# Kernel optimization log

Hardware: AMD Instinct MI355X
Metric: run time of the kernel (lower is better)

The kernel has to match this reference:

```python
import jax, jax.numpy as jnp
import numpy as np

N = 50000
E = 800000
G = 2500  # number of graphs


def setup_inputs() -> dict:
    key = jax.random.key(0)
    ks = jax.random.split(key, 10)
    x = jax.random.normal(ks[0], (N, 128), dtype=jnp.float32)
    edge_index = jax.random.randint(ks[1], (2, E), 0, N, dtype=jnp.int64)
    batch = jnp.sort(jax.random.randint(ks[2], (N,), 0, G, dtype=jnp.int64))
    def lin(k, fan_in, shape):
        return jax.random.normal(k, shape, dtype=jnp.float32) / np.sqrt(fan_in)
    return {
        'x': x, 'edge_index': edge_index, 'batch': batch,
        'W1': lin(ks[3], 128, (128, 64)), 'b1': jnp.zeros((64,), jnp.float32),
        'W2': lin(ks[4], 64, (64, 64)),  'b2': jnp.zeros((64,), jnp.float32),
        'W3': lin(ks[5], 64, (64, 64)),  'b3': jnp.zeros((64,), jnp.float32),
        'Wp1': lin(ks[6], 64, (64, 64)), 'bp1': jnp.zeros((64,), jnp.float32),
        'Wp2': lin(ks[7], 64, (64, 32)), 'bp2': jnp.zeros((32,), jnp.float32),
    }


def _gcn_norm(edge_index, n_nodes):
    # PyG GCNConv default: add self-loops, symmetric normalization
    loops = jnp.arange(n_nodes, dtype=edge_index.dtype)
    src = jnp.concatenate([edge_index[0], loops])
    dst = jnp.concatenate([edge_index[1], loops])
    deg = jax.ops.segment_sum(jnp.ones_like(dst, dtype=jnp.float32), dst,
                              num_segments=n_nodes)
    dis = jnp.where(deg > 0, jax.lax.rsqrt(deg), 0.0)
    norm = dis[src] * dis[dst]  # [E + N]
    return src, dst, norm


def _gcn_conv(x, W, b, src, dst, norm, n_nodes):
    h = x @ W                                   # transform first (small dim)
    m = h[src] * norm[:, None]                  # gather + scale
    out = jax.ops.segment_sum(m, dst, num_segments=n_nodes)  # scatter-add
    return out + b


def reference(x, edge_index, batch, W1, b1, W2, b2, W3, b3, Wp1, bp1, Wp2, bp2):
    n_nodes = x.shape[0]
    src, dst, norm = _gcn_norm(edge_index, n_nodes)
    x1 = jax.nn.relu(_gcn_conv(x, W1, b1, src, dst, norm, n_nodes))
    x2 = jax.nn.relu(_gcn_conv(x1, W2, b2, src, dst, norm, n_nodes))
    x3 = jax.nn.relu(_gcn_conv(x2, W3, b3, src, dst, norm, n_nodes))
    h = x1 + x2 + x3
    # global_mean_pool
    sums = jax.ops.segment_sum(h, batch, num_segments=G)
    counts = jax.ops.segment_sum(jnp.ones((n_nodes,), jnp.float32), batch,
                                 num_segments=G)
    pooled = sums / jnp.maximum(counts, 1.0)[:, None]
    z = jax.nn.relu(pooled @ Wp1 + bp1) @ Wp2 + bp2
    return z
```

## Files before the change

kernel.cpp:

```cpp
#include <hip/hip_runtime.h>
#include <math.h>


typedef short short8 __attribute__((ext_vector_type(8)));
typedef float f32x4 __attribute__((ext_vector_type(4)));

__device__ inline float bf2f(unsigned short h) {
    return __uint_as_float((unsigned)h << 16);
}
__device__ inline unsigned short f2bf(float f) {
    unsigned u = __float_as_uint(f);
    return (unsigned short)((u + (0x7FFFu + ((u >> 16) & 1u))) >> 16);
}
__device__ inline void bh8f(short8 u, float4& a, float4& b) {
    a.x = bf2f((unsigned short)u[0]); a.y = bf2f((unsigned short)u[1]);
    a.z = bf2f((unsigned short)u[2]); a.w = bf2f((unsigned short)u[3]);
    b.x = bf2f((unsigned short)u[4]); b.y = bf2f((unsigned short)u[5]);
    b.z = bf2f((unsigned short)u[6]); b.w = bf2f((unsigned short)u[7]);
}
__device__ inline float4 f4add(float4 a, float4 acc) {
    acc.x += a.x; acc.y += a.y; acc.z += a.z; acc.w += a.w;
    return acc;
}

template <int K>
__global__ __launch_bounds__(256) void k_hist_gemm(const int* __restrict__ dst,
                                                   int* __restrict__ hist, int E, int chunk,
                                                   const float* __restrict__ X,
                                                   const float* __restrict__ W,
                                                   unsigned short* __restrict__ H, int n) {
    __shared__ int hh[256];
    __shared__ short wt[64 * K];
    int t = threadIdx.x;
    if (blockIdx.x < 256) {
        hh[t] = 0;
        __syncthreads();
        int e0 = blockIdx.x * chunk;
        int e1 = min(e0 + chunk, E);
        for (int e = e0 + t; e < e1; e += 256) atomicAdd(&hh[dst[e] >> 8], 1);
        __syncthreads();
        hist[blockIdx.x * 256 + t] = hh[t];
        return;
    }
    for (int idx = t; idx < 64 * K; idx += 256) {
        int k = idx >> 6, ch = idx & 63;
        wt[ch * K + k] = (short)f2bf(W[idx]);
    }
    __syncthreads();
    int wave = t >> 6, lane = t & 63;
    int q = lane >> 4, l = lane & 15;
    int tile = (blockIdx.x - 256) * 4 + wave;
    if (tile * 16 >= n) return;
    int node = tile * 16 + l;
    short8 afr[4][K / 32];
#pragma unroll
    for (int mb = 0; mb < 4; mb++)
#pragma unroll
        for (int s = 0; s < K / 32; s++)
            afr[mb][s] = *(const short8*)(wt + (mb * 16 + l) * K + s * 32 + q * 8);
    f32x4 acc[4] = {};
    const float* xr = X + (size_t)node * K + q * 8;
#pragma unroll
    for (int s = 0; s < K / 32; s++) {
        float4 xa = *(const float4*)(xr + s * 32);
        float4 xb = *(const float4*)(xr + s * 32 + 4);
        short8 bfr;
        bfr[0] = (short)f2bf(xa.x); bfr[1] = (short)f2bf(xa.y);
        bfr[2] = (short)f2bf(xa.z); bfr[3] = (short)f2bf(xa.w);
        bfr[4] = (short)f2bf(xb.x); bfr[5] = (short)f2bf(xb.y);
        bfr[6] = (short)f2bf(xb.z); bfr[7] = (short)f2bf(xb.w);
#pragma unroll
        for (int mb = 0; mb < 4; mb++)
            acc[mb] = __builtin_amdgcn_mfma_f32_16x16x32_bf16(afr[mb][s], bfr, acc[mb], 0, 0, 0);
    }
#pragma unroll
    for (int mb = 0; mb < 4; mb++) {
        ushort4 u;
        u.x = f2bf(acc[mb][0]); u.y = f2bf(acc[mb][1]);
        u.z = f2bf(acc[mb][2]); u.w = f2bf(acc[mb][3]);
        ((ushort4*)H)[(size_t)node * 16 + mb * 4 + q] = u;
    }
}

__global__ void kA_colscan(const int* __restrict__ hist, int* __restrict__ cursorA,
                           int* __restrict__ tot) {
    __shared__ int s[256];
    int t = threadIdx.x;
    int k = blockIdx.x;
    int v = hist[t * 256 + k];
    s[t] = v;
    __syncthreads();
    for (int st = 1; st < 256; st <<= 1) {
        int u = s[t];
        if (t >= st) u += s[t - st];
        __syncthreads();
        s[t] = u;
        __syncthreads();
    }
    cursorA[t * 256 + k] = s[t] - v;
    if (t == 255) tot[k] = s[255];
}

__global__ void kA_scatter(const int* __restrict__ src, const int* __restrict__ dst,
                           const int* __restrict__ cursorA, const int* __restrict__ tot,
                           unsigned* __restrict__ ebuf, int E, int chunk) {
    __shared__ int s[256];
    __shared__ int cur[256];
    int t = threadIdx.x;
    s[t] = tot[t];
    __syncthreads();
    for (int st = 1; st < 256; st <<= 1) {
        int u = s[t];
        if (t >= st) u += s[t - st];
        __syncthreads();
        s[t] = u;
        __syncthreads();
    }
    int bstart = (t == 0) ? 0 : s[t - 1];
    cur[t] = cursorA[blockIdx.x * 256 + t] + bstart;
    __syncthreads();
    int e0 = blockIdx.x * chunk;
    int e1 = min(e0 + chunk, E);
    for (int e = e0 + t; e < e1; e += 256) {
        int d = dst[e];
        int p = atomicAdd(&cur[d >> 8], 1);
        ebuf[p] = ((unsigned)(d & 255) << 24) | (unsigned)src[e];
    }
}

__global__ void kB(const unsigned* __restrict__ ebuf, const int* __restrict__ tot,
                   float* __restrict__ dis, int* __restrict__ offsP,
                   unsigned* __restrict__ col, unsigned short* __restrict__ Hb,
                   unsigned short* __restrict__ Hb2, int N, int ZR) {
    __shared__ int s[256];
    __shared__ int h[256];
    __shared__ int cur[256];
    __shared__ float sdis[256];
    int t = threadIdx.x;
    int k = blockIdx.x;
    s[t] = tot[t];
    __syncthreads();
    for (int st = 1; st < 256; st <<= 1) {
        int u = s[t];
        if (t >= st) u += s[t - st];
        __syncthreads();
        s[t] = u;
        __syncthreads();
    }
    int lo = (k == 0) ? 0 : s[k - 1];
    int hi = s[k];
    int padbase = ((lo + 3) & ~3) + 768 * k;
    h[t] = 0;
    __syncthreads();
    for (int p = lo + t; p < hi; p += 256) atomicAdd(&h[ebuf[p] >> 24], 1);
    __syncthreads();
    int c = h[t];
    int cp = (c + 3) & ~3;
    int node = k * 256 + t;
    float dn = rsqrtf((float)(c + 1));
    sdis[t] = dn;
    if (node < N) dis[node] = dn;
    s[t] = cp;
    __syncthreads();
    for (int st = 1; st < 256; st <<= 1) {
        int u = s[t];
        if (t >= st) u += s[t - st];
        __syncthreads();
        s[t] = u;
        __syncthreads();
    }
    int start = padbase + s[t] - cp;
    if (node < N) offsP[node] = (start << 9) | cp;
    cur[t] = start;
    __syncthreads();
    for (int p = lo + t; p < hi; p += 256) {
        unsigned e = ebuf[p];
        int q = atomicAdd(&cur[e >> 24], 1);
        col[q] = e & 0x00FFFFFFu;
    }
    __syncthreads();
    if (node < N) {
        int end = start + cp;
        for (int q = cur[t]; q < end; q++) col[q] = (unsigned)ZR;
    }
    for (int idx = t; idx < 2048; idx += 256) {
        int nl = idx >> 3, cs = idx & 7;
        int nd = k * 256 + nl;
        if (nd >= N) continue;
        float d2 = sdis[nl];
        short8 v = ((const short8*)Hb)[(size_t)nd * 8 + cs];
        float4 a, b;
        bh8f(v, a, b);
        short8 o;
        o[0] = (short)f2bf(a.x * d2); o[1] = (short)f2bf(a.y * d2);
        o[2] = (short)f2bf(a.z * d2); o[3] = (short)f2bf(a.w * d2);
        o[4] = (short)f2bf(b.x * d2); o[5] = (short)f2bf(b.y * d2);
        o[6] = (short)f2bf(b.z * d2); o[7] = (short)f2bf(b.w * d2);
        ((short8*)Hb)[(size_t)nd * 8 + cs] = o;
    }
    if (k == 0) {
        if (t < 32) ((unsigned*)Hb)[(size_t)ZR * 32 + t] = 0u;
        else if (t < 64) ((unsigned*)Hb2)[(size_t)ZR * 32 + (t - 32)] = 0u;
    }
}

__global__ __launch_bounds__(256) void k_aggemm(const unsigned short* __restrict__ H,
                                                const unsigned* __restrict__ col,
                                                const int* __restrict__ offsP,
                                                const float* __restrict__ dis,
                                                const float* __restrict__ bias,
                                                const float* __restrict__ W,
                                                unsigned short* __restrict__ Xout,
                                                unsigned short* __restrict__ Hout, int n) {
    __shared__ short wt[64 * 64];
    __shared__ short vbuf[32 * 72];
    int t = threadIdx.x;
    for (int idx = t; idx < 64 * 64; idx += 256) {
        int k = idx >> 6, ch = idx & 63;
        wt[ch * 64 + k] = (short)f2bf(W[idx]);
    }
    const short8* Hs = (const short8*)H;
    int base = blockIdx.x * 32;
    int cs = t & 7;
    int nl = t >> 3;
    int node = base + nl;
    const float4* bias4 = (const float4*)bias;
    float4 bb0 = bias4[cs * 2];
    float4 bb1 = bias4[cs * 2 + 1];
    if (node < n) {
        float dn = dis[node];
        float4 acc0, acc1;
        bh8f(Hs[(size_t)node * 8 + cs], acc0, acc1);
        int po = offsP[node];
        int p = po >> 9, hiP = p + (po & 511);
        for (; p + 8 <= hiP; p += 8) {
            uint4 ea = *(const uint4*)(col + p);
            uint4 eb = *(const uint4*)(col + p + 4);
            short8 g0 = Hs[(size_t)ea.x * 8 + cs];
            short8 g1 = Hs[(size_t)ea.y * 8 + cs];
            short8 g2 = Hs[(size_t)ea.z * 8 + cs];
            short8 g3 = Hs[(size_t)ea.w * 8 + cs];
            short8 g4 = Hs[(size_t)eb.x * 8 + cs];
            short8 g5 = Hs[(size_t)eb.y * 8 + cs];
            short8 g6 = Hs[(size_t)eb.z * 8 + cs];
            short8 g7 = Hs[(size_t)eb.w * 8 + cs];
            float4 a, b;
            bh8f(g0, a, b); acc0 = f4add(a, acc0); acc1 = f4add(b, acc1);
            bh8f(g1, a, b); acc0 = f4add(a, acc0); acc1 = f4add(b, acc1);
            bh8f(g2, a, b); acc0 = f4add(a, acc0); acc1 = f4add(b, acc1);
            bh8f(g3, a, b); acc0 = f4add(a, acc0); acc1 = f4add(b, acc1);
            bh8f(g4, a, b); acc0 = f4add(a, acc0); acc1 = f4add(b, acc1);
            bh8f(g5, a, b); acc0 = f4add(a, acc0); acc1 = f4add(b, acc1);
            bh8f(g6, a, b); acc0 = f4add(a, acc0); acc1 = f4add(b, acc1);
            bh8f(g7, a, b); acc0 = f4add(a, acc0); acc1 = f4add(b, acc1);
        }
        if (p < hiP) {
            uint4 e4 = *(const uint4*)(col + p);
            short8 g0 = Hs[(size_t)e4.x * 8 + cs];
            short8 g1 = Hs[(size_t)e4.y * 8 + cs];
            short8 g2 = Hs[(size_t)e4.z * 8 + cs];
            short8 g3 = Hs[(size_t)e4.w * 8 + cs];
            float4 a, b;
            bh8f(g0, a, b); acc0 = f4add(a, acc0); acc1 = f4add(b, acc1);
            bh8f(g1, a, b); acc0 = f4add(a, acc0); acc1 = f4add(b, acc1);
            bh8f(g2, a, b); acc0 = f4add(a, acc0); acc1 = f4add(b, acc1);
            bh8f(g3, a, b); acc0 = f4add(a, acc0); acc1 = f4add(b, acc1);
        }
        float4 v0, v1;
        v0.x = fmaxf(acc0.x * dn + bb0.x, 0.f);
        v0.y = fmaxf(acc0.y * dn + bb0.y, 0.f);
        v0.z = fmaxf(acc0.z * dn + bb0.z, 0.f);
        v0.w = fmaxf(acc0.w * dn + bb0.w, 0.f);
        v1.x = fmaxf(acc1.x * dn + bb1.x, 0.f);
        v1.y = fmaxf(acc1.y * dn + bb1.y, 0.f);
        v1.z = fmaxf(acc1.z * dn + bb1.z, 0.f);
        v1.w = fmaxf(acc1.w * dn + bb1.w, 0.f);
        short8 o;
        o[0] = (short)f2bf(v0.x); o[1] = (short)f2bf(v0.y);
        o[2] = (short)f2bf(v0.z); o[3] = (short)f2bf(v0.w);
        o[4] = (short)f2bf(v1.x); o[5] = (short)f2bf(v1.y);
        o[6] = (short)f2bf(v1.z); o[7] = (short)f2bf(v1.w);
        ((short8*)Xout)[(size_t)node * 8 + cs] = o;
        *(short8*)(vbuf + nl * 72 + cs * 8) = o;
    }
    __syncthreads();
    int wave = t >> 6, lane = t & 63;
    if (wave >= 2) return;
    int q = lane >> 4, l = lane & 15;
    if (base + wave * 16 >= n) return;
    int mnode = base + wave * 16 + l;
    float dn2 = dis[mnode];
    short8 afr[4][2];
#pragma unroll
    for (int mb = 0; mb < 4; mb++)
#pragma unroll
        for (int s = 0; s < 2; s++)
            afr[mb][s] = *(const short8*)(wt + (mb * 16 + l) * 64 + s * 32 + q * 8);
    f32x4 acc[4] = {};
#pragma unroll
    for (int s = 0; s < 2; s++) {
        short8 bfr = *(const short8*)(vbuf + (wave * 16 + l) * 72 + s * 32 + q * 8);
#pragma unroll
        for (int mb = 0; mb < 4; mb++)
            acc[mb] = __builtin_amdgcn_mfma_f32_16x16x32_bf16(afr[mb][s], bfr, acc[mb], 0, 0, 0);
    }
#pragma unroll
    for (int mb = 0; mb < 4; mb++) {
        ushort4 u;
        u.x = f2bf(acc[mb][0] * dn2); u.y = f2bf(acc[mb][1] * dn2);
        u.z = f2bf(acc[mb][2] * dn2); u.w = f2bf(acc[mb][3] * dn2);
        ((ushort4*)Hout)[(size_t)mnode * 16 + mb * 4 + q] = u;
    }
}

__global__ void k_agg3(const unsigned short* __restrict__ H, const unsigned* __restrict__ col,
                       const int* __restrict__ offsP, const float* __restrict__ dis,
                       const float* __restrict__ bias,
                       const unsigned short* __restrict__ add1,
                       const unsigned short* __restrict__ add2,
                       float* __restrict__ OutS, int n) {
    int t = threadIdx.x;
    int node = blockIdx.x * 32 + (t >> 3);
    if (node >= n) return;
    int lane = t & 7;
    const short8* Hs = (const short8*)H;
    float dn = dis[node];
    float4 acc0, acc1;
    bh8f(Hs[(size_t)node * 8 + lane], acc0, acc1);
    int po = offsP[node];
    int p = po >> 9, hiP = p + (po & 511);
    for (; p + 8 <= hiP; p += 8) {
        uint4 ea = *(const uint4*)(col + p);
        uint4 eb = *(const uint4*)(col + p + 4);
        short8 g0 = Hs[(size_t)ea.x * 8 + lane];
        short8 g1 = Hs[(size_t)ea.y * 8 + lane];
        short8 g2 = Hs[(size_t)ea.z * 8 + lane];
        short8 g3 = Hs[(size_t)ea.w * 8 + lane];
        short8 g4 = Hs[(size_t)eb.x * 8 + lane];
        short8 g5 = Hs[(size_t)eb.y * 8 + lane];
        short8 g6 = Hs[(size_t)eb.z * 8 + lane];
        short8 g7 = Hs[(size_t)eb.w * 8 + lane];
        float4 a, b;
        bh8f(g0, a, b); acc0 = f4add(a, acc0); acc1 = f4add(b, acc1);
        bh8f(g1, a, b); acc0 = f4add(a, acc0); acc1 = f4add(b, acc1);
        bh8f(g2, a, b); acc0 = f4add(a, acc0); acc1 = f4add(b, acc1);
        bh8f(g3, a, b); acc0 = f4add(a, acc0); acc1 = f4add(b, acc1);
        bh8f(g4, a, b); acc0 = f4add(a, acc0); acc1 = f4add(b, acc1);
        bh8f(g5, a, b); acc0 = f4add(a, acc0); acc1 = f4add(b, acc1);
        bh8f(g6, a, b); acc0 = f4add(a, acc0); acc1 = f4add(b, acc1);
        bh8f(g7, a, b); acc0 = f4add(a, acc0); acc1 = f4add(b, acc1);
    }
    if (p < hiP) {
        uint4 e4 = *(const uint4*)(col + p);
        short8 g0 = Hs[(size_t)e4.x * 8 + lane];
        short8 g1 = Hs[(size_t)e4.y * 8 + lane];
        short8 g2 = Hs[(size_t)e4.z * 8 + lane];
        short8 g3 = Hs[(size_t)e4.w * 8 + lane];
        float4 a, b;
        bh8f(g0, a, b); acc0 = f4add(a, acc0); acc1 = f4add(b, acc1);
        bh8f(g1, a, b); acc0 = f4add(a, acc0); acc1 = f4add(b, acc1);
        bh8f(g2, a, b); acc0 = f4add(a, acc0); acc1 = f4add(b, acc1);
        bh8f(g3, a, b); acc0 = f4add(a, acc0); acc1 = f4add(b, acc1);
    }
    const float4* bias4 = (const float4*)bias;
    float4 bb0 = bias4[lane * 2];
    float4 bb1 = bias4[lane * 2 + 1];
    float4 v0, v1;
    v0.x = fmaxf(acc0.x * dn + bb0.x, 0.f);
    v0.y = fmaxf(acc0.y * dn + bb0.y, 0.f);
    v0.z = fmaxf(acc0.z * dn + bb0.z, 0.f);
    v0.w = fmaxf(acc0.w * dn + bb0.w, 0.f);
    v1.x = fmaxf(acc1.x * dn + bb1.x, 0.f);
    v1.y = fmaxf(acc1.y * dn + bb1.y, 0.f);
    v1.z = fmaxf(acc1.z * dn + bb1.z, 0.f);
    v1.w = fmaxf(acc1.w * dn + bb1.w, 0.f);
    size_t slot = (size_t)node * 8 + lane;
    float4 a10, a11, a20, a21;
    bh8f(((const short8*)add1)[slot], a10, a11);
    bh8f(((const short8*)add2)[slot], a20, a21);
    v0.x += a10.x + a20.x; v0.y += a10.y + a20.y;
    v0.z += a10.z + a20.z; v0.w += a10.w + a20.w;
    v1.x += a11.x + a21.x; v1.y += a11.y + a21.y;
    v1.z += a11.z + a21.z; v1.w += a11.w + a21.w;
    float4* S4 = (float4*)OutS;
    size_t oi = (size_t)node * 16 + (size_t)lane * 2;
    S4[oi] = v0;
    S4[oi + 1] = v1;
}

__global__ void k_poolhead(const float* __restrict__ S, const int* __restrict__ batch,
                           const float* __restrict__ Wp1, const float* __restrict__ bp1,
                           const float* __restrict__ Wp2, const float* __restrict__ bp2,
                           float* __restrict__ out, int n, int G) {
    int g = blockIdx.x;
    int j = threadIdx.x;
    int a = 0, b = n;
    while (a < b) { int m = (a + b) >> 1; if (batch[m] < g) a = m + 1; else b = m; }
    int beg = a;
    b = n;
    while (a < b) { int m = (a + b) >> 1; if (batch[m] < g + 1) a = m + 1; else b = m; }
    int end = a;
    float sum = 0.f;
    int i = beg;
    for (; i + 2 <= end; i += 2)
        sum += S[(size_t)i * 64 + j] + S[(size_t)(i + 1) * 64 + j];
    if (i < end) sum += S[(size_t)i * 64 + j];
    float cnt = (float)(end - beg);
    float p = sum / fmaxf(cnt, 1.f);
    __shared__ float ps[64];
    __shared__ float ts[64];
    ps[j] = p;
    __syncthreads();
    float t1 = bp1[j];
#pragma unroll 8
    for (int k = 0; k < 64; k++) t1 += ps[k] * Wp1[k * 64 + j];
    t1 = fmaxf(t1, 0.f);
    ts[j] = t1;
    __syncthreads();
    if (j < 32) {
        float o = bp2[j];
#pragma unroll 8
        for (int k = 0; k < 64; k++) o += ts[k] * Wp2[k * 32 + j];
        out[(size_t)g * 32 + j] = o;
    }
}

extern "C" void kernel_launch(void* const* d_in, const int* in_sizes, int n_in,
                              void* d_out, int out_size, void* d_ws, size_t ws_size,
                              hipStream_t stream) {
    const float* x   = (const float*)d_in[0];
    const int*   ei  = (const int*)d_in[1];
    const int*   bat = (const int*)d_in[2];
    const float* W1  = (const float*)d_in[3];
    const float* b1  = (const float*)d_in[4];
    const float* W2  = (const float*)d_in[5];
    const float* b2  = (const float*)d_in[6];
    const float* W3  = (const float*)d_in[7];
    const float* b3  = (const float*)d_in[8];
    const float* Wp1 = (const float*)d_in[9];
    const float* bp1 = (const float*)d_in[10];
    const float* Wp2 = (const float*)d_in[11];
    const float* bp2 = (const float*)d_in[12];

    int N = in_sizes[0] / 128;
    int E = in_sizes[1] / 2;
    int G = out_size / 32;
    const int* src = ei;
    const int* dst = ei + E;

    char* w = (char*)d_ws;
    auto alloc = [&](size_t bytes) -> void* {
        void* p = (void*)w;
        w += (bytes + 255) & ~(size_t)255;
        return p;
    };
    int NB = (N + 255) / 256;
    int ZR = N;
    int*            offsP   = (int*)alloc((size_t)N * 4);
    unsigned*       col     = (unsigned*)alloc(((size_t)E + 3 * (size_t)N + 2048) * 4);
    float*          dis     = (float*)alloc((size_t)N * 4);
    int*            hist    = (int*)alloc((size_t)256 * 256 * 4);
    int*            cursorA = (int*)alloc((size_t)256 * 256 * 4);
    int*            tot     = (int*)alloc((size_t)256 * 4);
    unsigned*       ebuf    = (unsigned*)alloc((size_t)E * 4);
    unsigned short* Hb      = (unsigned short*)alloc(((size_t)N + 16) * 64 * 2);
    unsigned short* Hb2     = (unsigned short*)alloc(((size_t)N + 16) * 64 * 2);
    unsigned short* X1      = (unsigned short*)alloc((size_t)N * 64 * 2);
    unsigned short* X2      = (unsigned short*)alloc((size_t)N * 64 * 2);
    float*          S       = (float*)alloc((size_t)N * 64 * 4);

    int chunk = (E + 255) / 256;
    int ggemm = ((N >> 4) + 3) / 4;
    int gfuse = (N + 31) / 32;
    int gagg  = (N + 31) / 32;

    k_hist_gemm<128><<<256 + ggemm, 256, 0, stream>>>(dst, hist, E, chunk, x, W1, Hb, N);
    kA_colscan<<<256, 256, 0, stream>>>(hist, cursorA, tot);
    kA_scatter<<<256, 256, 0, stream>>>(src, dst, cursorA, tot, ebuf, E, chunk);
    kB<<<NB, 256, 0, stream>>>(ebuf, tot, dis, offsP, col, Hb, Hb2, N, ZR);

    k_aggemm<<<gfuse, 256, 0, stream>>>(Hb, col, offsP, dis, b1, W2, X1, Hb2, N);
    k_aggemm<<<gfuse, 256, 0, stream>>>(Hb2, col, offsP, dis, b2, W3, X2, Hb, N);
    k_agg3<<<gagg, 256, 0, stream>>>(Hb, col, offsP, dis, b3, X1, X2, S, N);

    k_poolhead<<<G, 64, 0, stream>>>(S, bat, Wp1, bp1, Wp2, bp2, (float*)d_out, N, G);
}
```

Measured before the change: 215.5 us.

## Merge preprocessing kernels into one cooperative kernel with grid syncs

Replaces the four CSR-build and first-GEMM kernels with a single cooperative kernel of 512 blocks that uses grid-wide syncs between the histogram/GEMM, column scan, scatter and bucket-sort phases. The aim is to remove kernel launch gaps and tail effects between the small preprocessing stages. The histogram now uses 512 edge chunks, and each scan thread handles two chunks. This adds the cost of grid barriers and needs all 512 blocks, each with 16KB of LDS for W1, to be co-resident.

```diff
diff --git a/kernel.cpp b/kernel.cpp
--- a/kernel.cpp
+++ b/kernel.cpp
@@ -1,4 +1,5 @@
 #include <hip/hip_runtime.h>
+#include <hip/hip_cooperative_groups.h>
 #include <math.h>
 
 
@@ -23,184 +24,180 @@
     return acc;
 }
 
-template <int K>
-__global__ __launch_bounds__(256) void k_hist_gemm(const int* __restrict__ dst,
-                                                   int* __restrict__ hist, int E, int chunk,
-                                                   const float* __restrict__ X,
-                                                   const float* __restrict__ W,
-                                                   unsigned short* __restrict__ H, int n) {
-    __shared__ int hh[256];
-    __shared__ short wt[64 * K];
-    int t = threadIdx.x;
-    if (blockIdx.x < 256) {
-        hh[t] = 0;
-        __syncthreads();
-        int e0 = blockIdx.x * chunk;
-        int e1 = min(e0 + chunk, E);
-        for (int e = e0 + t; e < e1; e += 256) atomicAdd(&hh[dst[e] >> 8], 1);
-        __syncthreads();
-        hist[blockIdx.x * 256 + t] = hh[t];
-        return;
-    }
-    for (int idx = t; idx < 64 * K; idx += 256) {
-        int k = idx >> 6, ch = idx & 63;
-        wt[ch * K + k] = (short)f2bf(W[idx]);
-    }
-    __syncthreads();
-    int wave = t >> 6, lane = t & 63;
-    int q = lane >> 4, l = lane & 15;
-    int tile = (blockIdx.x - 256) * 4 + wave;
-    if (tile * 16 >= n) return;
-    int node = tile * 16 + l;
-    short8 afr[4][K / 32];
-#pragma unroll
-    for (int mb = 0; mb < 4; mb++)
-#pragma unroll
-        for (int s = 0; s < K / 32; s++)
-            afr[mb][s] = *(const short8*)(wt + (mb * 16 + l) * K + s * 32 + q * 8);
-    f32x4 acc[4] = {};
-    const float* xr = X + (size_t)node * K + q * 8;
-#pragma unroll
-    for (int s = 0; s < K / 32; s++) {
-        float4 xa = *(const float4*)(xr + s * 32);
-        float4 xb = *(const float4*)(xr + s * 32 + 4);
-        short8 bfr;
-        bfr[0] = (short)f2bf(xa.x); bfr[1] = (short)f2bf(xa.y);
-        bfr[2] = (short)f2bf(xa.z); bfr[3] = (short)f2bf(xa.w);
-        bfr[4] = (short)f2bf(xb.x); bfr[5] = (short)f2bf(xb.y);
-        bfr[6] = (short)f2bf(xb.z); bfr[7] = (short)f2bf(xb.w);
-#pragma unroll
-        for (int mb = 0; mb < 4; mb++)
-            acc[mb] = __builtin_amdgcn_mfma_f32_16x16x32_bf16(afr[mb][s], bfr, acc[mb], 0, 0, 0);
-    }
-#pragma unroll
-    for (int mb = 0; mb < 4; mb++) {
-        ushort4 u;
-        u.x = f2bf(acc[mb][0]); u.y = f2bf(acc[mb][1]);
-        u.z = f2bf(acc[mb][2]); u.w = f2bf(acc[mb][3]);
-        ((ushort4*)H)[(size_t)node * 16 + mb * 4 + q] = u;
-    }
-}
-
-__global__ void kA_colscan(const int* __restrict__ hist, int* __restrict__ cursorA,
-                           int* __restrict__ tot) {
-    __shared__ int s[256];
-    int t = threadIdx.x;
-    int k = blockIdx.x;
-    int v = hist[t * 256 + k];
-    s[t] = v;
-    __syncthreads();
-    for (int st = 1; st < 256; st <<= 1) {
-        int u = s[t];
-        if (t >= st) u += s[t - st];
-        __syncthreads();
-        s[t] = u;
-        __syncthreads();
-    }
-    cursorA[t * 256 + k] = s[t] - v;
-    if (t == 255) tot[k] = s[255];
-}
-
-__global__ void kA_scatter(const int* __restrict__ src, const int* __restrict__ dst,
-                           const int* __restrict__ cursorA, const int* __restrict__ tot,
-                           unsigned* __restrict__ ebuf, int E, int chunk) {
-    __shared__ int s[256];
-    __shared__ int cur[256];
-    int t = threadIdx.x;
-    s[t] = tot[t];
-    __syncthreads();
-    for (int st = 1; st < 256; st <<= 1) {
-        int u = s[t];
-        if (t >= st) u += s[t - st];
-        __syncthreads();
-        s[t] = u;
-        __syncthreads();
-    }
-    int bstart = (t == 0) ? 0 : s[t - 1];
-    cur[t] = cursorA[blockIdx.x * 256 + t] + bstart;
-    __syncthreads();
-    int e0 = blockIdx.x * chunk;
-    int e1 = min(e0 + chunk, E);
-    for (int e = e0 + t; e < e1; e += 256) {
-        int d = dst[e];
-        int p = atomicAdd(&cur[d >> 8], 1);
-        ebuf[p] = ((unsigned)(d & 255) << 24) | (unsigned)src[e];
-    }
-}
-
-__global__ void kB(const unsigned* __restrict__ ebuf, const int* __restrict__ tot,
-                   float* __restrict__ dis, int* __restrict__ offsP,
-                   unsigned* __restrict__ col, unsigned short* __restrict__ Hb,
-                   unsigned short* __restrict__ Hb2, int N, int ZR) {
-    __shared__ int s[256];
-    __shared__ int h[256];
+__global__ __launch_bounds__(256) void k_pre(
+    const int* __restrict__ src, const int* __restrict__ dst, int E, int chunk,
+    const float* __restrict__ X, const float* __restrict__ W1,
+    unsigned short* __restrict__ Hb, unsigned short* __restrict__ Hb2,
+    int* __restrict__ hist, int* __restrict__ cursorA, int* __restrict__ tot,
+    unsigned* __restrict__ ebuf, float* __restrict__ dis, int* __restrict__ offsP,
+    unsigned* __restrict__ col, int N, int ZR, int nunits) {
+    __shared__ short wt[64 * 128];
+    __shared__ int sh[256];
+    __shared__ int h2[256];
     __shared__ int cur[256];
     __shared__ float sdis[256];
     int t = threadIdx.x;
-    int k = blockIdx.x;
-    s[t] = tot[t];
+    int b = blockIdx.x;
+    int NBLK = (int)gridDim.x;
+
+    for (int idx = t; idx < 64 * 128; idx += 256) {
+        int k = idx >> 6, ch = idx & 63;
+        wt[ch * 128 + k] = (short)f2bf(W1[idx]);
+    }
+    sh[t] = 0;
     __syncthreads();
-    for (int st = 1; st < 256; st <<= 1) {
-        int u = s[t];
-        if (t >= st) u += s[t - st];
-        __syncthreads();
-        s[t] = u;
-        __syncthreads();
-    }
-    int lo = (k == 0) ? 0 : s[k - 1];
-    int hi = s[k];
-    int padbase = ((lo + 3) & ~3) + 768 * k;
-    h[t] = 0;
+    int e0 = b * chunk;
+    int e1 = min(e0 + chunk, E);
+    for (int e = e0 + t; e < e1; e += 256) atomicAdd(&sh[dst[e] >> 8], 1);
     __syncthreads();
-    for (int p = lo + t; p < hi; p += 256) atomicAdd(&h[ebuf[p] >> 24], 1);
-    __syncthreads();
-    int c = h[t];
-    int cp = (c + 3) & ~3;
-    int node = k * 256 + t;
-    float dn = rsqrtf((float)(c + 1));
-    sdis[t] = dn;
-    if (node < N) dis[node] = dn;
-    s[t] = cp;
-    __syncthreads();
-    for (int st = 1; st < 256; st <<= 1) {
-        int u = s[t];
-        if (t >= st) u += s[t - st];
-        __syncthreads();
-        s[t] = u;
-        __syncthreads();
-    }
-    int start = padbase + s[t] - cp;
-    if (node < N) offsP[node] = (start << 9) | cp;
-    cur[t] = start;
-    __syncthreads();
-    for (int p = lo + t; p < hi; p += 256) {
-        unsigned e = ebuf[p];
-        int q = atomicAdd(&cur[e >> 24], 1);
-        col[q] = e & 0x00FFFFFFu;
-    }
-    __syncthreads();
-    if (node < N) {
-        int end = start + cp;
-        for (int q = cur[t]; q < end; q++) col[q] = (unsigned)ZR;
-    }
-    for (int idx = t; idx < 2048; idx += 256) {
-        int nl = idx >> 3, cs = idx & 7;
-        int nd = k * 256 + nl;
-        if (nd >= N) continue;
-        float d2 = sdis[nl];
-        short8 v = ((const short8*)Hb)[(size_t)nd * 8 + cs];
-        float4 a, b;
-        bh8f(v, a, b);
-        short8 o;
-        o[0] = (short)f2bf(a.x * d2); o[1] = (short)f2bf(a.y * d2);
-        o[2] = (short)f2bf(a.z * d2); o[3] = (short)f2bf(a.w * d2);
-        o[4] = (short)f2bf(b.x * d2); o[5] = (short)f2bf(b.y * d2);
-        o[6] = (short)f2bf(b.z * d2); o[7] = (short)f2bf(b.w * d2);
-        ((short8*)Hb)[(size_t)nd * 8 + cs] = o;
-    }
-    if (k == 0) {
-        if (t < 32) ((unsigned*)Hb)[(size_t)ZR * 32 + t] = 0u;
-        else if (t < 64) ((unsigned*)Hb2)[(size_t)ZR * 32 + (t - 32)] = 0u;
+    hist[b * 256 + t] = sh[t];
+    {
+        int wave = t >> 6, lane = t & 63;
+        int q = lane >> 4, l = lane & 15;
+        for (int unit = b; unit < nunits; unit += NBLK) {
+            int tile = unit * 4 + wave;
+            if (tile * 16 < N) {
+                int node = tile * 16 + l;
+                short8 afr[4][4];
+#pragma unroll
+                for (int mb = 0; mb < 4; mb++)
+#pragma unroll
+                    for (int s = 0; s < 4; s++)
+                        afr[mb][s] = *(const short8*)(wt + (mb * 16 + l) * 128 + s * 32 + q * 8);
+                f32x4 acc[4] = {};
+                const float* xr = X + (size_t)node * 128 + q * 8;
+#pragma unroll
+                for (int s = 0; s < 4; s++) {
+                    float4 xa = *(const float4*)(xr + s * 32);
+                    float4 xb = *(const float4*)(xr + s * 32 + 4);
+                    short8 bfr;
+                    bfr[0] = (short)f2bf(xa.x); bfr[1] = (short)f2bf(xa.y);
+                    bfr[2] = (short)f2bf(xa.z); bfr[3] = (short)f2bf(xa.w);
+                    bfr[4] = (short)f2bf(xb.x); bfr[5] = (short)f2bf(xb.y);
+                    bfr[6] = (short)f2bf(xb.z); bfr[7] = (short)f2bf(xb.w);
+#pragma unroll
+                    for (int mb = 0; mb < 4; mb++)
+                        acc[mb] = __builtin_amdgcn_mfma_f32_16x16x32_bf16(afr[mb][s], bfr, acc[mb], 0, 0, 0);
+                }
+#pragma unroll
+                for (int mb = 0; mb < 4; mb++) {
+                    ushort4 u;
+                    u.x = f2bf(acc[mb][0]); u.y = f2bf(acc[mb][1]);
+                    u.z = f2bf(acc[mb][2]); u.w = f2bf(acc[mb][3]);
+                    ((ushort4*)Hb)[(size_t)node * 16 + mb * 4 + q] = u;
+                }
+            }
+        }
+    }
+    cooperative_groups::this_grid().sync();
+
+    if (b < 256) {
+        int k = b;
+        int v0 = hist[(2 * t) * 256 + k];
+        int v1 = hist[(2 * t + 1) * 256 + k];
+        sh[t] = v0 + v1;
+        __syncthreads();
+        for (int st = 1; st < 256; st <<= 1) {
+            int u = sh[t];
+            if (t >= st) u += sh[t - st];
+            __syncthreads();
+            sh[t] = u;
+            __syncthreads();
+        }
+        int base0 = sh[t] - (v0 + v1);
+        cursorA[(2 * t) * 256 + k] = base0;
+        cursorA[(2 * t + 1) * 256 + k] = base0 + v0;
+        if (t == 255) tot[k] = sh[255];
+    }
+    cooperative_groups::this_grid().sync();
+
+    {
+        sh[t] = tot[t];
+        __syncthreads();
+        for (int st = 1; st < 256; st <<= 1) {
+            int u = sh[t];
+            if (t >= st) u += sh[t - st];
+            __syncthreads();
+            sh[t] = u;
+            __syncthreads();
+        }
+        int bstart = (t == 0) ? 0 : sh[t - 1];
+        cur[t] = cursorA[b * 256 + t] + bstart;
+        __syncthreads();
+        for (int e = e0 + t; e < e1; e += 256) {
+            int d = dst[e];
+            int p = atomicAdd(&cur[d >> 8], 1);
+            ebuf[p] = ((unsigned)(d & 255) << 24) | (unsigned)src[e];
+        }
+    }
+    cooperative_groups::this_grid().sync();
+
+    if (b * 256 >= N) return;
+    {
+        int k = b;
+        sh[t] = tot[t];
+        h2[t] = 0;
+        __syncthreads();
+        for (int st = 1; st < 256; st <<= 1) {
+            int u = sh[t];
+            if (t >= st) u += sh[t - st];
+            __syncthreads();
+            sh[t] = u;
+            __syncthreads();
+        }
+        int lo = (k == 0) ? 0 : sh[k - 1];
+        int hi = sh[k];
+        int padbase = ((lo + 3) & ~3) + 768 * k;
+        for (int p = lo + t; p < hi; p += 256) atomicAdd(&h2[ebuf[p] >> 24], 1);
+        __syncthreads();
+        int c = h2[t];
+        int cp = (c + 3) & ~3;
+        int node = k * 256 + t;
+        float dn = rsqrtf((float)(c + 1));
+        sdis[t] = dn;
+        if (node < N) dis[node] = dn;
+        sh[t] = cp;
+        __syncthreads();
+        for (int st = 1; st < 256; st <<= 1) {
+            int u = sh[t];
+            if (t >= st) u += sh[t - st];
+            __syncthreads();
+            sh[t] = u;
+            __syncthreads();
+        }
+        int start = padbase + sh[t] - cp;
+        if (node < N) offsP[node] = (start << 9) | cp;
+        cur[t] = start;
+        __syncthreads();
+        for (int p = lo + t; p < hi; p += 256) {
+            unsigned e = ebuf[p];
+            int q = atomicAdd(&cur[e >> 24], 1);
+            col[q] = e & 0x00FFFFFFu;
+        }
+        __syncthreads();
+        if (node < N) {
+            int end = start + cp;
+            for (int q = cur[t]; q < end; q++) col[q] = (unsigned)ZR;
+        }
+        for (int idx = t; idx < 2048; idx += 256) {
+            int nl = idx >> 3, cs = idx & 7;
+            int nd = k * 256 + nl;
+            if (nd >= N) continue;
+            float d2 = sdis[nl];
+            short8 v = ((const short8*)Hb)[(size_t)nd * 8 + cs];
+            float4 a, bb;
+            bh8f(v, a, bb);
+            short8 o;
+            o[0] = (short)f2bf(a.x * d2); o[1] = (short)f2bf(a.y * d2);
+            o[2] = (short)f2bf(a.z * d2); o[3] = (short)f2bf(a.w * d2);
+            o[4] = (short)f2bf(bb.x * d2); o[5] = (short)f2bf(bb.y * d2);
+            o[6] = (short)f2bf(bb.z * d2); o[7] = (short)f2bf(bb.w * d2);
+            ((short8*)Hb)[(size_t)nd * 8 + cs] = o;
+        }
+        if (k == 0) {
+            if (t < 32) ((unsigned*)Hb)[(size_t)ZR * 32 + t] = 0u;
+            else if (t < 64) ((unsigned*)Hb2)[(size_t)ZR * 32 + (t - 32)] = 0u;
+        }
     }
 }
 
@@ -454,13 +451,12 @@
         w += (bytes + 255) & ~(size_t)255;
         return p;
     };
-    int NB = (N + 255) / 256;
     int ZR = N;
     int*            offsP   = (int*)alloc((size_t)N * 4);
     unsigned*       col     = (unsigned*)alloc(((size_t)E + 3 * (size_t)N + 2048) * 4);
     float*          dis     = (float*)alloc((size_t)N * 4);
-    int*            hist    = (int*)alloc((size_t)256 * 256 * 4);
-    int*            cursorA = (int*)alloc((size_t)256 * 256 * 4);
+    int*            hist    = (int*)alloc((size_t)512 * 256 * 4);
+    int*            cursorA = (int*)alloc((size_t)512 * 256 * 4);
     int*            tot     = (int*)alloc((size_t)256 * 4);
     unsigned*       ebuf    = (unsigned*)alloc((size_t)E * 4);
     unsigned short* Hb      = (unsigned short*)alloc(((size_t)N + 16) * 64 * 2);
@@ -469,15 +465,20 @@
     unsigned short* X2      = (unsigned short*)alloc((size_t)N * 64 * 2);
     float*          S       = (float*)alloc((size_t)N * 64 * 4);
 
-    int chunk = (E + 255) / 256;
-    int ggemm = ((N >> 4) + 3) / 4;
+    int chunk = (E + 511) / 512;
+    int nunits = (N + 63) / 64;
     int gfuse = (N + 31) / 32;
     int gagg  = (N + 31) / 32;
 
-    k_hist_gemm<128><<<256 + ggemm, 256, 0, stream>>>(dst, hist, E, chunk, x, W1, Hb, N);
-    kA_colscan<<<256, 256, 0, stream>>>(hist, cursorA, tot);
-    kA_scatter<<<256, 256, 0, stream>>>(src, dst, cursorA, tot, ebuf, E, chunk);
-    kB<<<NB, 256, 0, stream>>>(ebuf, tot, dis, offsP, col, Hb, Hb2, N, ZR);
+    {
+        void* args[] = {(void*)&src, (void*)&dst, (void*)&E, (void*)&chunk,
+                        (void*)&x, (void*)&W1, (void*)&Hb, (void*)&Hb2,
+                        (void*)&hist, (void*)&cursorA, (void*)&tot,
+                        (void*)&ebuf, (void*)&dis, (void*)&offsP, (void*)&col,
+                        (void*)&N, (void*)&ZR, (void*)&nunits};
+        hipLaunchCooperativeKernel((const void*)k_pre, dim3(512), dim3(256),
+                                   args, 0, stream);
+    }
 
     k_aggemm<<<gfuse, 256, 0, stream>>>(Hb, col, offsP, dis, b1, W2, X1, Hb2, N);
     k_aggemm<<<gfuse, 256, 0, stream>>>(Hb2, col, offsP, dis, b2, W3, X2, Hb, N);
```

After: 409.5 us. 90.0% more time.

## Fuse mean-pool accumulation into final aggregation kernel via segmented atomics

Applied to the files above, without the earlier changes.

The last GCN aggregation now reduces its per-node outputs within each 32-node block by graph id in shared memory and atomically adds partial sums into a small pooled buffer. This removes the full N×64 fp32 intermediate write and the later re-read in the pooling kernel. The pooled buffer is zeroed inside the column-scan kernel, so no extra launch is needed. It adds float atomics, which make the summation order nondeterministic, and a serial 32-step loop over the block's nodes run by 64 threads after a barrier.

```diff
diff --git a/kernel.cpp b/kernel.cpp
--- a/kernel.cpp
+++ b/kernel.cpp
@@ -83,7 +83,7 @@
 }
 
 __global__ void kA_colscan(const int* __restrict__ hist, int* __restrict__ cursorA,
-                           int* __restrict__ tot) {
+                           int* __restrict__ tot, float* __restrict__ pooled, int PG) {
     __shared__ int s[256];
     int t = threadIdx.x;
     int k = blockIdx.x;
@@ -99,6 +99,7 @@
     }
     cursorA[t * 256 + k] = s[t] - v;
     if (t == 255) tot[k] = s[255];
+    for (int i = k * 256 + t; i < PG; i += 65536) pooled[i] = 0.f;
 }
 
 __global__ void kA_scatter(const int* __restrict__ src, const int* __restrict__ dst,
@@ -313,85 +314,107 @@
     }
 }
 
-__global__ void k_agg3(const unsigned short* __restrict__ H, const unsigned* __restrict__ col,
-                       const int* __restrict__ offsP, const float* __restrict__ dis,
-                       const float* __restrict__ bias,
-                       const unsigned short* __restrict__ add1,
-                       const unsigned short* __restrict__ add2,
-                       float* __restrict__ OutS, int n) {
+__global__ __launch_bounds__(256) void k_agg3pool(const unsigned short* __restrict__ H,
+                                                  const unsigned* __restrict__ col,
+                                                  const int* __restrict__ offsP,
+                                                  const float* __restrict__ dis,
+                                                  const float* __restrict__ bias,
+                                                  const unsigned short* __restrict__ add1,
+                                                  const unsigned short* __restrict__ add2,
+                                                  const int* __restrict__ batch,
+                                                  float* __restrict__ pooled, int n) {
+    __shared__ float sm[32][65];
+    __shared__ int sg[32];
     int t = threadIdx.x;
-    int node = blockIdx.x * 32 + (t >> 3);
-    if (node >= n) return;
-    int lane = t & 7;
-    const short8* Hs = (const short8*)H;
-    float dn = dis[node];
-    float4 acc0, acc1;
-    bh8f(Hs[(size_t)node * 8 + lane], acc0, acc1);
-    int po = offsP[node];
-    int p = po >> 9, hiP = p + (po & 511);
-    for (; p + 8 <= hiP; p += 8) {
-        uint4 ea = *(const uint4*)(col + p);
-        uint4 eb = *(const uint4*)(col + p + 4);
-        short8 g0 = Hs[(size_t)ea.x * 8 + lane];
-        short8 g1 = Hs[(size_t)ea.y * 8 + lane];
-        short8 g2 = Hs[(size_t)ea.z * 8 + lane];
-        short8 g3 = Hs[(size_t)ea.w * 8 + lane];
-        short8 g4 = Hs[(size_t)eb.x * 8 + lane];
-        short8 g5 = Hs[(size_t)eb.y * 8 + lane];
-        short8 g6 = Hs[(size_t)eb.z * 8 + lane];
-        short8 g7 = Hs[(size_t)eb.w * 8 + lane];
-        float4 a, b;
-        bh8f(g0, a, b); acc0 = f4add(a, acc0); acc1 = f4add(b, acc1);
-        bh8f(g1, a, b); acc0 = f4add(a, acc0); acc1 = f4add(b, acc1);
-        bh8f(g2, a, b); acc0 = f4add(a, acc0); acc1 = f4add(b, acc1);
-        bh8f(g3, a, b); acc0 = f4add(a, acc0); acc1 = f4add(b, acc1);
-        bh8f(g4, a, b); acc0 = f4add(a, acc0); acc1 = f4add(b, acc1);
-        bh8f(g5, a, b); acc0 = f4add(a, acc0); acc1 = f4add(b, acc1);
-        bh8f(g6, a, b); acc0 = f4add(a, acc0); acc1 = f4add(b, acc1);
-        bh8f(g7, a, b); acc0 = f4add(a, acc0); acc1 = f4add(b, acc1);
-    }
-    if (p < hiP) {
-        uint4 e4 = *(const uint4*)(col + p);
-        short8 g0 = Hs[(size_t)e4.x * 8 + lane];
-        short8 g1 = Hs[(size_t)e4.y * 8 + lane];
-        short8 g2 = Hs[(size_t)e4.z * 8 + lane];
-        short8 g3 = Hs[(size_t)e4.w * 8 + lane];
-        float4 a, b;
-        bh8f(g0, a, b); acc0 = f4add(a, acc0); acc1 = f4add(b, acc1);
-        bh8f(g1, a, b); acc0 = f4add(a, acc0); acc1 = f4add(b, acc1);
-        bh8f(g2, a, b); acc0 = f4add(a, acc0); acc1 = f4add(b, acc1);
-        bh8f(g3, a, b); acc0 = f4add(a, acc0); acc1 = f4add(b, acc1);
-    }
-    const float4* bias4 = (const float4*)bias;
-    float4 bb0 = bias4[lane * 2];
-    float4 bb1 = bias4[lane * 2 + 1];
-    float4 v0, v1;
-    v0.x = fmaxf(acc0.x * dn + bb0.x, 0.f);
-    v0.y = fmaxf(acc0.y * dn + bb0.y, 0.f);
-    v0.z = fmaxf(acc0.z * dn + bb0.z, 0.f);
-    v0.w = fmaxf(acc0.w * dn + bb0.w, 0.f);
-    v1.x = fmaxf(acc1.x * dn + bb1.x, 0.f);
-    v1.y = fmaxf(acc1.y * dn + bb1.y, 0.f);
-    v1.z = fmaxf(acc1.z * dn + bb1.z, 0.f);
-    v1.w = fmaxf(acc1.w * dn + bb1.w, 0.f);
-    size_t slot = (size_t)node * 8 + lane;
-    float4 a10, a11, a20, a21;
-    bh8f(((const short8*)add1)[slot], a10, a11);
-    bh8f(((const short8*)add2)[slot], a20, a21);
-    v0.x += a10.x + a20.x; v0.y += a10.y + a20.y;
-    v0.z += a10.z + a20.z; v0.w += a10.w + a20.w;
-    v1.x += a11.x + a21.x; v1.y += a11.y + a21.y;
-    v1.z += a11.z + a21.z; v1.w += a11.w + a21.w;
-    float4* S4 = (float4*)OutS;
-    size_t oi = (size_t)node * 16 + (size_t)lane * 2;
-    S4[oi] = v0;
-    S4[oi + 1] = v1;
-}
-
-__global__ void k_poolhead(const float* __restrict__ S, const int* __restrict__ batch,
-                           const float* __restrict__ Wp1, const float* __restrict__ bp1,
-                           const float* __restrict__ Wp2, const float* __restrict__ bp2,
-                           float* __restrict__ out, int n, int G) {
+    int base = blockIdx.x * 32;
+    int nl = t >> 3, lane = t & 7;
+    int node = base + nl;
+    if (t < 32) sg[t] = (base + t < n) ? batch[base + t] : -1;
+    if (node < n) {
+        const short8* Hs = (const short8*)H;
+        float dn = dis[node];
+        float4 acc0, acc1;
+        bh8f(Hs[(size_t)node * 8 + lane], acc0, acc1);
+        int po = offsP[node];
+        int p = po >> 9, hiP = p + (po & 511);
+        for (; p + 8 <= hiP; p += 8) {
+            uint4 ea = *(const uint4*)(col + p);
+            uint4 eb = *(const uint4*)(col + p + 4);
+            short8 g0 = Hs[(size_t)ea.x * 8 + lane];
+            short8 g1 = Hs[(size_t)ea.y * 8 + lane];
+            short8 g2 = Hs[(size_t)ea.z * 8 + lane];
+            short8 g3 = Hs[(size_t)ea.w * 8 + lane];
+            short8 g4 = Hs[(size_t)eb.x * 8 + lane];
+            short8 g5 = Hs[(size_t)eb.y * 8 + lane];
+            short8 g6 = Hs[(size_t)eb.z * 8 + lane];
+            short8 g7 = Hs[(size_t)eb.w * 8 + lane];
+            float4 a, b;
+            bh8f(g0, a, b); acc0 = f4add(a, acc0); acc1 = f4add(b, acc1);
+            bh8f(g1, a, b); acc0 = f4add(a, acc0); acc1 = f4add(b, acc1);
+            bh8f(g2, a, b); acc0 = f4add(a, acc0); acc1 = f4add(b, acc1);
+            bh8f(g3, a, b); acc0 = f4add(a, acc0); acc1 = f4add(b, acc1);
+            bh8f(g4, a, b); acc0 = f4add(a, acc0); acc1 = f4add(b, acc1);
+            bh8f(g5, a, b); acc0 = f4add(a, acc0); acc1 = f4add(b, acc1);
+            bh8f(g6, a, b); acc0 = f4add(a, acc0); acc1 = f4add(b, acc1);
+            bh8f(g7, a, b); acc0 = f4add(a, acc0); acc1 = f4add(b, acc1);
+        }
+        if (p < hiP) {
+            uint4 e4 = *(const uint4*)(col + p);
+            short8 g0 = Hs[(size_t)e4.x * 8 + lane];
+            short8 g1 = Hs[(size_t)e4.y * 8 + lane];
+            short8 g2 = Hs[(size_t)e4.z * 8 + lane];
+            short8 g3 = Hs[(size_t)e4.w * 8 + lane];
+            float4 a, b;
+            bh8f(g0, a, b); acc0 = f4add(a, acc0); acc1 = f4add(b, acc1);
+            bh8f(g1, a, b); acc0 = f4add(a, acc0); acc1 = f4add(b, acc1);
+            bh8f(g2, a, b); acc0 = f4add(a, acc0); acc1 = f4add(b, acc1);
+            bh8f(g3, a, b); acc0 = f4add(a, acc0); acc1 = f4add(b, acc1);
+        }
+        const float4* bias4 = (const float4*)bias;
+        float4 bb0 = bias4[lane * 2];
+        float4 bb1 = bias4[lane * 2 + 1];
+        float4 v0, v1;
+        v0.x = fmaxf(acc0.x * dn + bb0.x, 0.f);
+        v0.y = fmaxf(acc0.y * dn + bb0.y, 0.f);
+        v0.z = fmaxf(acc0.z * dn + bb0.z, 0.f);
+        v0.w = fmaxf(acc0.w * dn + bb0.w, 0.f);
+        v1.x = fmaxf(acc1.x * dn + bb1.x, 0.f);
+        v1.y = fmaxf(acc1.y * dn + bb1.y, 0.f);
+        v1.z = fmaxf(acc1.z * dn + bb1.z, 0.f);
+        v1.w = fmaxf(acc1.w * dn + bb1.w, 0.f);
+        size_t slot = (size_t)node * 8 + lane;
+        float4 a10, a11, a20, a21;
+        bh8f(((const short8*)add1)[slot], a10, a11);
+        bh8f(((const short8*)add2)[slot], a20, a21);
+        v0.x += a10.x + a20.x; v0.y += a10.y + a20.y;
+        v0.z += a10.z + a20.z; v0.w += a10.w + a20.w;
+        v1.x += a11.x + a21.x; v1.y += a11.y + a21.y;
+        v1.z += a11.z + a21.z; v1.w += a11.w + a21.w;
+        float* r = &sm[nl][lane * 8];
+        r[0] = v0.x; r[1] = v0.y; r[2] = v0.z; r[3] = v0.w;
+        r[4] = v1.x; r[5] = v1.y; r[6] = v1.z; r[7] = v1.w;
+    }
+    __syncthreads();
+    if (t < 64) {
+        float acc = 0.f;
+        int cg = -1;
+        for (int i = 0; i < 32; i++) {
+            int g = sg[i];
+            if (g != cg) {
+                if (cg >= 0) atomicAdd(&pooled[(size_t)cg * 64 + t], acc);
+                cg = g;
+                acc = 0.f;
+            }
+            if (g >= 0) acc += sm[i][t];
+        }
+        if (cg >= 0) atomicAdd(&pooled[(size_t)cg * 64 + t], acc);
+    }
+}
+
+__global__ void k_head(const float* __restrict__ pooled, const int* __restrict__ batch,
+                       const float* __restrict__ Wp1, const float* __restrict__ bp1,
+                       const float* __restrict__ Wp2, const float* __restrict__ bp2,
+                       float* __restrict__ out, int n, int G) {
     int g = blockIdx.x;
     int j = threadIdx.x;
     int a = 0, b = n;
@@ -400,13 +423,8 @@
     b = n;
     while (a < b) { int m = (a + b) >> 1; if (batch[m] < g + 1) a = m + 1; else b = m; }
     int end = a;
-    float sum = 0.f;
-    int i = beg;
-    for (; i + 2 <= end; i += 2)
-        sum += S[(size_t)i * 64 + j] + S[(size_t)(i + 1) * 64 + j];
-    if (i < end) sum += S[(size_t)i * 64 + j];
     float cnt = (float)(end - beg);
-    float p = sum / fmaxf(cnt, 1.f);
+    float p = pooled[(size_t)g * 64 + j] / fmaxf(cnt, 1.f);
     __shared__ float ps[64];
     __shared__ float ts[64];
     ps[j] = p;
@@ -467,7 +485,7 @@
     unsigned short* Hb2     = (unsigned short*)alloc(((size_t)N + 16) * 64 * 2);
     unsigned short* X1      = (unsigned short*)alloc((size_t)N * 64 * 2);
     unsigned short* X2      = (unsigned short*)alloc((size_t)N * 64 * 2);
-    float*          S       = (float*)alloc((size_t)N * 64 * 4);
+    float*          pooled  = (float*)alloc((size_t)G * 64 * 4);
 
     int chunk = (E + 255) / 256;
     int ggemm = ((N >> 4) + 3) / 4;
@@ -475,13 +493,13 @@
     int gagg  = (N + 31) / 32;
 
     k_hist_gemm<128><<<256 + ggemm, 256, 0, stream>>>(dst, hist, E, chunk, x, W1, Hb, N);
-    kA_colscan<<<256, 256, 0, stream>>>(hist, cursorA, tot);
+    kA_colscan<<<256, 256, 0, stream>>>(hist, cursorA, tot, pooled, G * 64);
     kA_scatter<<<256, 256, 0, stream>>>(src, dst, cursorA, tot, ebuf, E, chunk);
     kB<<<NB, 256, 0, stream>>>(ebuf, tot, dis, offsP, col, Hb, Hb2, N, ZR);
 
     k_aggemm<<<gfuse, 256, 0, stream>>>(Hb, col, offsP, dis, b1, W2, X1, Hb2, N);
     k_aggemm<<<gfuse, 256, 0, stream>>>(Hb2, col, offsP, dis, b2, W3, X2, Hb, N);
-    k_agg3<<<gagg, 256, 0, stream>>>(Hb, col, offsP, dis, b3, X1, X2, S, N);
-
-    k_poolhead<<<G, 64, 0, stream>>>(S, bat, Wp1, bp1, Wp2, bp2, (float*)d_out, N, G);
-}
+    k_agg3pool<<<gagg, 256, 0, stream>>>(Hb, col, offsP, dis, b3, X1, X2, bat, pooled, N);
+
+    k_head<<<G, 64, 0, stream>>>(pooled, bat, Wp1, bp1, Wp2, bp2, (float*)d_out, N, G);
+}
```

After: 209.8 us (median of 2 runs). 2.7% less time.
